# Kernel tuning notes

Measured on AMD Instinct MI355X. Metric: run time of the kernel, lower is better.

## Reference

```python
import jax, jax.numpy as jnp
import numpy as np

B, S, H, D = 2, 8192, 16, 64
P = 8            # lsh_num_projs
BS = 256         # block_size
SAMP = 256       # sample_size


def _gray_perm(num_projs):
    # AngularLSH._unit_hamming_distance_array: maps bin ids to Gray-code order
    a = np.array([0, 1], dtype=np.int32)
    for _ in range(num_projs - 1):
        a = np.concatenate([a, np.flip(a) + a.shape[0]])
    return a

_PERM = jnp.asarray(_gray_perm(P))          # (2**P,)
_POW2 = jnp.asarray(2 ** np.arange(P), dtype=jnp.int32)


def setup_inputs() -> dict:
    rng = jax.random.key(0)
    k1, k2, k3, k4, k5 = jax.random.split(rng, 5)
    return {
        "query": jax.random.normal(k1, (B, S, H, D), jnp.float32),
        "key": jax.random.normal(k2, (B, S, H, D), jnp.float32),
        "value": jax.random.normal(k3, (B, S, H, D), jnp.float32),
        "proj_dir": jax.random.normal(k4, (D, P), jnp.float32),
        "sample_idx": jax.random.randint(k5, (B, H, SAMP), 0, S),
    }


def _lsh_hash(x, proj_dir):
    # x: (B,S,H,D) -> Gray-coded bucket ids (B,H,S)
    bits = (jnp.einsum("bshd,dp->bhsp", x, proj_dir) > 0).astype(jnp.int32)
    bins = (bits * _POW2).sum(-1)
    return _PERM[bins]


def _gather_seq(x, idx_bhs):
    # x: (B,S,H,...) gathered along seq by idx (B,H,S)
    idx = jnp.transpose(idx_bhs, (0, 2, 1))  # (B,S,H)
    if x.ndim == 4:
        idx = idx[..., None]
    return jnp.take_along_axis(x, idx, axis=1)


def reference(query, key, value, proj_dir, sample_idx):
    scale = 1.0 / float(np.sqrt(D))
    nb = S // BS

    # --- LSH sort of queries and keys (stable argsort over seq) ---
    q_sort = jnp.argsort(_lsh_hash(query, proj_dir), axis=2)   # (B,H,S)
    k_sort = jnp.argsort(_lsh_hash(key, proj_dir), axis=2)     # (B,H,S)

    q_s = _gather_seq(query, q_sort)   # (B,S,H,D)
    k_s = _gather_seq(key, k_sort)
    v_s = _gather_seq(value, k_sort)

    # --- block-diagonal attention in sorted order ---
    qb = q_s.reshape(B, nb, BS, H, D)
    kb = k_s.reshape(B, nb, BS, H, D)
    vb = v_s.reshape(B, nb, BS, H, D)
    s_blk = jnp.einsum("bnihd,bnjhd->bhnij", qb, kb) * scale   # (B,H,nb,BS,BS)
    lse_blk = jax.nn.logsumexp(s_blk, axis=-1)                 # (B,H,nb,BS)
    a_blk = jnp.einsum("bhnij,bnjhd->bnihd", jax.nn.softmax(s_blk, axis=-1), vb)
    a_blk = a_blk.reshape(B, S, H, D)                          # sorted order
    lse_blk = jnp.transpose(lse_blk, (0, 2, 3, 1)).reshape(B, S, H)

    # un-sort back to original query order
    q_inv = jnp.argsort(q_sort, axis=2)                        # inverse perm (B,H,S)
    a_blk = _gather_seq(a_blk, q_inv)                          # (B,S,H,D)
    lse_blk = _gather_seq(lse_blk, q_inv)                      # (B,S,H)

    # --- residual: uniform sampled-key attention with importance weight ---
    k_r = _gather_seq(key, sample_idx)                         # (B,SAMP,H,D)
    v_r = _gather_seq(value, sample_idx)
    s_r = jnp.einsum("bihd,bjhd->bhij", query, k_r) * scale    # (B,H,S,SAMP)
    lse_r = jax.nn.logsumexp(s_r, axis=-1) + jnp.log(S / SAMP) # (B,H,S)
    a_r = jnp.einsum("bhij,bjhd->bihd", jax.nn.softmax(s_r, axis=-1), v_r)
    lse_r = jnp.transpose(lse_r, (0, 2, 1))                    # (B,S,H)

    # --- combine block + residual estimates via log-sum-exp ---
    lse_t = jnp.logaddexp(lse_blk, lse_r)                      # (B,S,H)
    w_blk = jnp.exp(lse_blk - lse_t)[..., None]
    w_r = jnp.exp(lse_r - lse_t)[..., None]
    attn = a_blk * w_blk + a_r * w_r                           # (B,S,H,D)
    return attn
```

## Files before the change

kernel.cpp:

```cpp
#include <hip/hip_runtime.h>
#include <hip/hip_bf16.h>

#define B 2
#define S 8192
#define H 16
#define D 64
#define NB 32
#define BS 256
#define SAMP 256
#define BH (B*H)
#define BHS (B*H*S)
#define BSHD (B*S*H*D)
#define LOG32 3.4657359027997265f

typedef float f32x4 __attribute__((ext_vector_type(4)));
typedef short bf16x8 __attribute__((ext_vector_type(8)));

__device__ __forceinline__ unsigned short f2bf(float x) {
    unsigned int u = __builtin_bit_cast(unsigned int, x);
    u += 0x7fffu + ((u >> 16) & 1u);
    return (unsigned short)(u >> 16);
}
__device__ __forceinline__ unsigned int pack2(float a, float b) {
    return (unsigned int)f2bf(a) | ((unsigned int)f2bf(b) << 16);
}

__global__ __launch_bounds__(256) void k_prep(const float* __restrict__ q,
                                              const float* __restrict__ k,
                                              const float* __restrict__ v,
                                              const float* __restrict__ pd,
                                              int* __restrict__ hq,
                                              int* __restrict__ hk,
                                              unsigned short* __restrict__ qbf,
                                              unsigned short* __restrict__ kbf,
                                              unsigned short* __restrict__ vbf) {
    __shared__ float spd[D * 8];
    const int t = threadIdx.x;
    for (int i = t; i < D * 8; i += 256) spd[i] = pd[i];
    __syncthreads();

    const int sc = blockIdx.x & (NB - 1);
    const int bh = blockIdx.x >> 5;
    const int s  = sc * 256 + t;
    const int h  = bh & (H - 1), b = bh >> 4;
    const int base = ((b * S + s) * H + h) << 6;

    float dq[8], dk[8];
#pragma unroll
    for (int p = 0; p < 8; ++p) { dq[p] = 0.f; dk[p] = 0.f; }

#pragma unroll
    for (int i = 0; i < 8; ++i) {
        float4 x0 = ((const float4*)(q + base + i * 8))[0];
        float4 x1 = ((const float4*)(q + base + i * 8))[1];
        float4 y0 = ((const float4*)(k + base + i * 8))[0];
        float4 y1 = ((const float4*)(k + base + i * 8))[1];
#pragma unroll
        for (int p = 0; p < 8; ++p) {
            dq[p] += x0.x * spd[(8*i+0)*8+p] + x0.y * spd[(8*i+1)*8+p]
                   + x0.z * spd[(8*i+2)*8+p] + x0.w * spd[(8*i+3)*8+p]
                   + x1.x * spd[(8*i+4)*8+p] + x1.y * spd[(8*i+5)*8+p]
                   + x1.z * spd[(8*i+6)*8+p] + x1.w * spd[(8*i+7)*8+p];
            dk[p] += y0.x * spd[(8*i+0)*8+p] + y0.y * spd[(8*i+1)*8+p]
                   + y0.z * spd[(8*i+2)*8+p] + y0.w * spd[(8*i+3)*8+p]
                   + y1.x * spd[(8*i+4)*8+p] + y1.y * spd[(8*i+5)*8+p]
                   + y1.z * spd[(8*i+6)*8+p] + y1.w * spd[(8*i+7)*8+p];
        }
        uint4 uq, uk;
        uq.x = pack2(x0.x * 0.125f, x0.y * 0.125f);
        uq.y = pack2(x0.z * 0.125f, x0.w * 0.125f);
        uq.z = pack2(x1.x * 0.125f, x1.y * 0.125f);
        uq.w = pack2(x1.z * 0.125f, x1.w * 0.125f);
        uk.x = pack2(y0.x, y0.y); uk.y = pack2(y0.z, y0.w);
        uk.z = pack2(y1.x, y1.y); uk.w = pack2(y1.z, y1.w);
        *(uint4*)(qbf + base + i * 8) = uq;
        *(uint4*)(kbf + base + i * 8) = uk;

        float4 z0 = ((const float4*)(v + base + i * 8))[0];
        float4 z1 = ((const float4*)(v + base + i * 8))[1];
        uint4 uv;
        uv.x = pack2(z0.x, z0.y); uv.y = pack2(z0.z, z0.w);
        uv.z = pack2(z1.x, z1.y); uv.w = pack2(z1.z, z1.w);
        *(uint4*)(vbf + base + i * 8) = uv;
    }
    int bq = 0, bk = 0;
#pragma unroll
    for (int p = 0; p < 8; ++p) {
        bq |= (dq[p] > 0.f) ? (1 << p) : 0;
        bk |= (dk[p] > 0.f) ? (1 << p) : 0;
    }
    hq[bh * S + s] = bq ^ (bq >> 1);
    hk[bh * S + s] = bk ^ (bk >> 1);
}

#define SORT_NT 64
#define SORT_CH (S / SORT_NT)

__global__ __launch_bounds__(SORT_NT) void k_sort(const int* __restrict__ hq,
                                                  const int* __restrict__ hk,
                                                  int* __restrict__ qs,
                                                  int* __restrict__ ks) {
    __shared__ int hist[SORT_NT * 256];
    __shared__ int base[257];
    const int t  = threadIdx.x;
    const int bh = blockIdx.x & (BH - 1);
    const bool isQ = blockIdx.x < BH;
    const int* hp = (isQ ? hq : hk) + bh * S;
    int*       sp = (isQ ? qs : ks) + bh * S;

    for (int i = 0; i < 256; ++i) hist[t * 256 + i] = 0;
    __syncthreads();
    for (int i = 0; i < SORT_CH; ++i) hist[t * 256 + hp[t * SORT_CH + i]]++;
    __syncthreads();

    for (int bi = 0; bi < 4; ++bi) {
        const int bin = t * 4 + bi;
        int sum = 0;
        for (int tt = 0; tt < SORT_NT; ++tt) sum += hist[tt * 256 + bin];
        base[bin + 1] = sum;
    }
    __syncthreads();
    if (t == 0) {
        base[0] = 0;
        for (int i = 1; i <= 256; ++i) base[i] += base[i - 1];
    }
    __syncthreads();

    for (int bi = 0; bi < 4; ++bi) {
        const int bin = t * 4 + bi;
        int run = base[bin];
        for (int tt = 0; tt < SORT_NT; ++tt) {
            int c = hist[tt * 256 + bin];
            hist[tt * 256 + bin] = run;
            run += c;
        }
    }
    __syncthreads();

    for (int i = 0; i < SORT_CH; ++i) {
        const int s0  = t * SORT_CH + i;
        const int bin = hp[s0];
        sp[hist[t * 256 + bin]++] = s0;
    }
}

#define VP 264
#define PP 40

__global__ __launch_bounds__(512, 4) void k_attn(const unsigned short* __restrict__ qbf,
                                                 const unsigned short* __restrict__ kbf,
                                                 const unsigned short* __restrict__ vbf,
                                                 const int* __restrict__ qs,
                                                 const int* __restrict__ ks,
                                                 const int* __restrict__ sidx,
                                                 float* __restrict__ out) {
    __shared__ __align__(16) unsigned short vT[64 * VP];
    __shared__ __align__(16) unsigned short pL[8 * 32 * PP];

    const int t    = threadIdx.x;
    const int w    = t >> 6;
    const int lane = t & 63;
    const int lg   = lane >> 4;
    const int lr   = lane & 15;
    const int blk  = blockIdx.x & (NB - 1);
    const int bh   = blockIdx.x >> 5;
    const int h    = bh & (H - 1), b = bh >> 4;
    const int sbase = bh * S + blk * BS;
    unsigned short* pw = pL + w * 32 * PP;

    int qrow[2]; bf16x8 bq[2][2];
#pragma unroll
    for (int qg = 0; qg < 2; ++qg) {
        qrow[qg] = qs[sbase + w * 32 + qg * 16 + lr];
        const unsigned short* qp = qbf + (((b * S + qrow[qg]) * H + h) << 6);
        bq[qg][0] = *(const bf16x8*)(qp + lg * 8);
        bq[qg][1] = *(const bf16x8*)(qp + 32 + lg * 8);
    }

    float m_run[2] = {-1e30f, -1e30f}, l_run[2] = {0.f, 0.f};
    f32x4 acc[2][4];
#pragma unroll
    for (int qg = 0; qg < 2; ++qg)
#pragma unroll
        for (int dg = 0; dg < 4; ++dg) acc[qg][dg] = (f32x4){0.f, 0.f, 0.f, 0.f};

    for (int pass = 0; pass < 2; ++pass) {
        if (pass) __syncthreads();
        {
            const int key = t >> 1, d0 = (t & 1) * 32;
            const int krow = pass ? sidx[bh * SAMP + key] : ks[sbase + key];
            const unsigned short* vp = vbf + (((b * S + krow) * H + h) << 6) + d0;
#pragma unroll
            for (int i = 0; i < 4; ++i) {
                uint4 x = *(const uint4*)(vp + i * 8);
                const int d = d0 + i * 8;
                vT[(d + 0) * VP + key] = (unsigned short)(x.x);
                vT[(d + 1) * VP + key] = (unsigned short)(x.x >> 16);
                vT[(d + 2) * VP + key] = (unsigned short)(x.y);
                vT[(d + 3) * VP + key] = (unsigned short)(x.y >> 16);
                vT[(d + 4) * VP + key] = (unsigned short)(x.z);
                vT[(d + 5) * VP + key] = (unsigned short)(x.z >> 16);
                vT[(d + 6) * VP + key] = (unsigned short)(x.w);
                vT[(d + 7) * VP + key] = (unsigned short)(x.w >> 16);
            }
        }
        __syncthreads();

        const float bias = pass ? LOG32 : 0.f;
        for (int kt4 = 0; kt4 < 4; ++kt4) {
            int krw[4];
#pragma unroll
            for (int kg = 0; kg < 4; ++kg) {
                const int key = kt4 * 64 + kg * 16 + lr;
                krw[kg] = pass ? sidx[bh * SAMP + key] : ks[sbase + key];
            }
            f32x4 c[2][4];
#pragma unroll
            for (int kf = 0; kf < 2; ++kf) {
                bf16x8 ak[4];
#pragma unroll
                for (int kg = 0; kg < 4; ++kg)
                    ak[kg] = *(const bf16x8*)(kbf + (((b * S + krw[kg]) * H + h) << 6)
                                              + kf * 32 + lg * 8);
#pragma unroll
                for (int qg = 0; qg < 2; ++qg)
#pragma unroll
                    for (int kg = 0; kg < 4; ++kg) {
                        f32x4 cin = kf ? c[qg][kg] : (f32x4){0.f, 0.f, 0.f, 0.f};
                        c[qg][kg] = __builtin_amdgcn_mfma_f32_16x16x32_bf16(ak[kg], bq[qg][kf], cin, 0, 0, 0);
                    }
            }
            float esc[2];
#pragma unroll
            for (int qg = 0; qg < 2; ++qg) {
                float tm = -1e30f;
#pragma unroll
                for (int kg = 0; kg < 4; ++kg)
#pragma unroll
                    for (int r = 0; r < 4; ++r) tm = fmaxf(tm, c[qg][kg][r]);
                tm = fmaxf(tm, __shfl_xor(tm, 16));
                tm = fmaxf(tm, __shfl_xor(tm, 32));
                tm += bias;
                const float mn = fmaxf(m_run[qg], tm);
                esc[qg] = __expf(m_run[qg] - mn);
                m_run[qg] = mn;
                const float mnb = mn - bias;
                float rs = 0.f;
#pragma unroll
                for (int kg = 0; kg < 4; ++kg)
#pragma unroll
                    for (int r = 0; r < 4; ++r) {
                        const float p = __expf(c[qg][kg][r] - mnb);
                        c[qg][kg][r] = p;
                        rs += p;
                    }
                rs += __shfl_xor(rs, 16);
                rs += __shfl_xor(rs, 32);
                l_run[qg] = l_run[qg] * esc[qg] + rs;
            }
#pragma unroll
            for (int qg = 0; qg < 2; ++qg)
#pragma unroll
                for (int r = 0; r < 4; ++r) {
                    const float er = __shfl(esc[qg], lg * 4 + r);
#pragma unroll
                    for (int dg = 0; dg < 4; ++dg) acc[qg][dg][r] *= er;
                }
#pragma unroll
            for (int hh = 0; hh < 2; ++hh) {
#pragma unroll
                for (int qg = 0; qg < 2; ++qg)
#pragma unroll
                    for (int kg2 = 0; kg2 < 2; ++kg2) {
                        const int kg = hh * 2 + kg2;
                        uint2 u;
                        u.x = pack2(c[qg][kg][0], c[qg][kg][1]);
                        u.y = pack2(c[qg][kg][2], c[qg][kg][3]);
                        *(uint2*)&pw[(qg * 16 + lr) * PP + kg2 * 16 + lg * 4] = u;
                    }
                bf16x8 bv[4];
#pragma unroll
                for (int dg = 0; dg < 4; ++dg)
                    bv[dg] = *(const bf16x8*)&vT[(dg * 16 + lr) * VP + kt4 * 64 + hh * 32 + lg * 8];
#pragma unroll
                for (int qg = 0; qg < 2; ++qg) {
                    const bf16x8 ap = *(const bf16x8*)&pw[(qg * 16 + lr) * PP + lg * 8];
#pragma unroll
                    for (int dg = 0; dg < 4; ++dg)
                        acc[qg][dg] = __builtin_amdgcn_mfma_f32_16x16x32_bf16(ap, bv[dg], acc[qg][dg], 0, 0, 0);
                }
            }
        }
    }

#pragma unroll
    for (int qg = 0; qg < 2; ++qg)
#pragma unroll
        for (int r = 0; r < 4; ++r) {
            const float lq = __shfl(l_run[qg], lg * 4 + r);
            const int   qr = __shfl(qrow[qg], lg * 4 + r);
            const float inv = 1.f / lq;
            const int obase = ((b * S + qr) * H + h) << 6;
#pragma unroll
            for (int dg = 0; dg < 4; ++dg)
                out[obase + dg * 16 + lr] = acc[qg][dg][r] * inv;
        }
}

extern "C" void kernel_launch(void* const* d_in, const int* in_sizes, int n_in,
                              void* d_out, int out_size, void* d_ws, size_t ws_size,
                              hipStream_t stream) {
    const float* q   = (const float*)d_in[0];
    const float* k   = (const float*)d_in[1];
    const float* v   = (const float*)d_in[2];
    const float* pd  = (const float*)d_in[3];
    const int*  sidx = (const int*)d_in[4];
    float* out = (float*)d_out;

    int* hq = (int*)d_ws;
    int* hk = hq + BHS;
    int* qs = hk + BHS;
    int* ks = qs + BHS;
    unsigned short* qbf = (unsigned short*)(ks + BHS);
    unsigned short* kbf = qbf + BSHD;
    unsigned short* vbf = kbf + BSHD;

    k_prep<<<BH * NB, 256, 0, stream>>>(q, k, v, pd, hq, hk, qbf, kbf, vbf);
    k_sort<<<2 * BH, SORT_NT, 0, stream>>>(hq, hk, qs, ks);
    k_attn<<<BH * NB, 512, 0, stream>>>(qbf, kbf, vbf, qs, ks, sidx, out);
}
```

Baseline: 230.4 us.

## Drop bf16 query staging, remap prep threads, lazy rescale, swizzle attention blocks

After: 379.4 us. 1.65x slower.

```diff
diff --git a/kernel.cpp b/kernel.cpp
--- a/kernel.cpp
+++ b/kernel.cpp
@@ -25,25 +25,25 @@
     return (unsigned int)f2bf(a) | ((unsigned int)f2bf(b) << 16);
 }
 
-__global__ __launch_bounds__(256) void k_prep(const float* __restrict__ q,
-                                              const float* __restrict__ k,
-                                              const float* __restrict__ v,
-                                              const float* __restrict__ pd,
-                                              int* __restrict__ hq,
-                                              int* __restrict__ hk,
-                                              unsigned short* __restrict__ qbf,
-                                              unsigned short* __restrict__ kbf,
-                                              unsigned short* __restrict__ vbf) {
+__global__ __launch_bounds__(256, 3) void k_prep(const float* __restrict__ q,
+                                                 const float* __restrict__ k,
+                                                 const float* __restrict__ v,
+                                                 const float* __restrict__ pd,
+                                                 int* __restrict__ hq,
+                                                 int* __restrict__ hk,
+                                                 unsigned short* __restrict__ kbf,
+                                                 unsigned short* __restrict__ vbf) {
     __shared__ float spd[D * 8];
+    __shared__ int   ht[2][16][16];
     const int t = threadIdx.x;
     for (int i = t; i < D * 8; i += 256) spd[i] = pd[i];
     __syncthreads();
 
-    const int sc = blockIdx.x & (NB - 1);
-    const int bh = blockIdx.x >> 5;
-    const int s  = sc * 256 + t;
-    const int h  = bh & (H - 1), b = bh >> 4;
-    const int base = ((b * S + s) * H + h) << 6;
+    const int b  = blockIdx.x >> 9;
+    const int s0 = (blockIdx.x & 511) * 16;
+    const int sl = t >> 4;
+    const int h  = t & 15;
+    const int base = ((b * S + s0 + sl) * H + h) << 6;
 
     float dq[8], dk[8];
 #pragma unroll
@@ -53,29 +53,26 @@
     for (int i = 0; i < 8; ++i) {
         float4 x0 = ((const float4*)(q + base + i * 8))[0];
         float4 x1 = ((const float4*)(q + base + i * 8))[1];
-        float4 y0 = ((const float4*)(k + base + i * 8))[0];
-        float4 y1 = ((const float4*)(k + base + i * 8))[1];
 #pragma unroll
         for (int p = 0; p < 8; ++p) {
             dq[p] += x0.x * spd[(8*i+0)*8+p] + x0.y * spd[(8*i+1)*8+p]
                    + x0.z * spd[(8*i+2)*8+p] + x0.w * spd[(8*i+3)*8+p]
                    + x1.x * spd[(8*i+4)*8+p] + x1.y * spd[(8*i+5)*8+p]
                    + x1.z * spd[(8*i+6)*8+p] + x1.w * spd[(8*i+7)*8+p];
+        }
+        float4 y0 = ((const float4*)(k + base + i * 8))[0];
+        float4 y1 = ((const float4*)(k + base + i * 8))[1];
+#pragma unroll
+        for (int p = 0; p < 8; ++p) {
             dk[p] += y0.x * spd[(8*i+0)*8+p] + y0.y * spd[(8*i+1)*8+p]
                    + y0.z * spd[(8*i+2)*8+p] + y0.w * spd[(8*i+3)*8+p]
                    + y1.x * spd[(8*i+4)*8+p] + y1.y * spd[(8*i+5)*8+p]
                    + y1.z * spd[(8*i+6)*8+p] + y1.w * spd[(8*i+7)*8+p];
         }
-        uint4 uq, uk;
-        uq.x = pack2(x0.x * 0.125f, x0.y * 0.125f);
-        uq.y = pack2(x0.z * 0.125f, x0.w * 0.125f);
-        uq.z = pack2(x1.x * 0.125f, x1.y * 0.125f);
-        uq.w = pack2(x1.z * 0.125f, x1.w * 0.125f);
+        uint4 uk;
         uk.x = pack2(y0.x, y0.y); uk.y = pack2(y0.z, y0.w);
         uk.z = pack2(y1.x, y1.y); uk.w = pack2(y1.z, y1.w);
-        *(uint4*)(qbf + base + i * 8) = uq;
         *(uint4*)(kbf + base + i * 8) = uk;
-
         float4 z0 = ((const float4*)(v + base + i * 8))[0];
         float4 z1 = ((const float4*)(v + base + i * 8))[1];
         uint4 uv;
@@ -89,8 +86,16 @@
         bq |= (dq[p] > 0.f) ? (1 << p) : 0;
         bk |= (dk[p] > 0.f) ? (1 << p) : 0;
     }
-    hq[bh * S + s] = bq ^ (bq >> 1);
-    hk[bh * S + s] = bk ^ (bk >> 1);
+    ht[0][h][sl] = bq ^ (bq >> 1);
+    ht[1][h][sl] = bk ^ (bk >> 1);
+    __syncthreads();
+
+    if (t < 128) {
+        const int inp = t >> 6, r = t & 63, h2 = r >> 2, p2 = r & 3;
+        int4 val = *(const int4*)&ht[inp][h2][p2 * 4];
+        int* dst = inp ? hk : hq;
+        *(int4*)&dst[(b * H + h2) * S + s0 + p2 * 4] = val;
+    }
 }
 
 #define SORT_NT 64
@@ -147,7 +152,7 @@
 #define VP 264
 #define PP 40
 
-__global__ __launch_bounds__(512, 4) void k_attn(const unsigned short* __restrict__ qbf,
+__global__ __launch_bounds__(512, 4) void k_attn(const float* __restrict__ q,
                                                  const unsigned short* __restrict__ kbf,
                                                  const unsigned short* __restrict__ vbf,
                                                  const int* __restrict__ qs,
@@ -162,8 +167,9 @@
     const int lane = t & 63;
     const int lg   = lane >> 4;
     const int lr   = lane & 15;
-    const int blk  = blockIdx.x & (NB - 1);
-    const int bh   = blockIdx.x >> 5;
+    const int logical = (blockIdx.x & 7) * (BH * NB / 8) + (blockIdx.x >> 3);
+    const int blk  = logical & (NB - 1);
+    const int bh   = logical >> 5;
     const int h    = bh & (H - 1), b = bh >> 4;
     const int sbase = bh * S + blk * BS;
     unsigned short* pw = pL + w * 32 * PP;
@@ -172,9 +178,18 @@
 #pragma unroll
     for (int qg = 0; qg < 2; ++qg) {
         qrow[qg] = qs[sbase + w * 32 + qg * 16 + lr];
-        const unsigned short* qp = qbf + (((b * S + qrow[qg]) * H + h) << 6);
-        bq[qg][0] = *(const bf16x8*)(qp + lg * 8);
-        bq[qg][1] = *(const bf16x8*)(qp + 32 + lg * 8);
+        const float* qp = q + (((b * S + qrow[qg]) * H + h) << 6);
+#pragma unroll
+        for (int kf = 0; kf < 2; ++kf) {
+            float4 x0 = ((const float4*)(qp + kf * 32 + lg * 8))[0];
+            float4 x1 = ((const float4*)(qp + kf * 32 + lg * 8))[1];
+            union { bf16x8 v8; unsigned int u[4]; } fa;
+            fa.u[0] = pack2(x0.x * 0.125f, x0.y * 0.125f);
+            fa.u[1] = pack2(x0.z * 0.125f, x0.w * 0.125f);
+            fa.u[2] = pack2(x1.x * 0.125f, x1.y * 0.125f);
+            fa.u[3] = pack2(x1.z * 0.125f, x1.w * 0.125f);
+            bq[qg][kf] = fa.v8;
+        }
     }
 
     float m_run[2] = {-1e30f, -1e30f}, l_run[2] = {0.f, 0.f};
@@ -230,7 +245,6 @@
                         c[qg][kg] = __builtin_amdgcn_mfma_f32_16x16x32_bf16(ak[kg], bq[qg][kf], cin, 0, 0, 0);
                     }
             }
-            float esc[2];
 #pragma unroll
             for (int qg = 0; qg < 2; ++qg) {
                 float tm = -1e30f;
@@ -241,10 +255,19 @@
                 tm = fmaxf(tm, __shfl_xor(tm, 16));
                 tm = fmaxf(tm, __shfl_xor(tm, 32));
                 tm += bias;
-                const float mn = fmaxf(m_run[qg], tm);
-                esc[qg] = __expf(m_run[qg] - mn);
-                m_run[qg] = mn;
-                const float mnb = mn - bias;
+                if (!__all(tm <= m_run[qg] + 8.f)) {
+                    const float mn  = fmaxf(m_run[qg], tm);
+                    const float es  = __expf(m_run[qg] - mn);
+                    m_run[qg] = mn;
+                    l_run[qg] *= es;
+#pragma unroll
+                    for (int r = 0; r < 4; ++r) {
+                        const float er = __shfl(es, lg * 4 + r);
+#pragma unroll
+                        for (int dg = 0; dg < 4; ++dg) acc[qg][dg][r] *= er;
+                    }
+                }
+                const float mnb = m_run[qg] - bias;
                 float rs = 0.f;
 #pragma unroll
                 for (int kg = 0; kg < 4; ++kg)
@@ -256,16 +279,8 @@
                     }
                 rs += __shfl_xor(rs, 16);
                 rs += __shfl_xor(rs, 32);
-                l_run[qg] = l_run[qg] * esc[qg] + rs;
-            }
-#pragma unroll
-            for (int qg = 0; qg < 2; ++qg)
-#pragma unroll
-                for (int r = 0; r < 4; ++r) {
-                    const float er = __shfl(esc[qg], lg * 4 + r);
-#pragma unroll
-                    for (int dg = 0; dg < 4; ++dg) acc[qg][dg][r] *= er;
-                }
+                l_run[qg] += rs;
+            }
 #pragma unroll
             for (int hh = 0; hh < 2; ++hh) {
 #pragma unroll
@@ -321,11 +336,10 @@
     int* hk = hq + BHS;
     int* qs = hk + BHS;
     int* ks = qs + BHS;
-    unsigned short* qbf = (unsigned short*)(ks + BHS);
-    unsigned short* kbf = qbf + BSHD;
+    unsigned short* kbf = (unsigned short*)(ks + BHS);
     unsigned short* vbf = kbf + BSHD;
 
-    k_prep<<<BH * NB, 256, 0, stream>>>(q, k, v, pd, hq, hk, qbf, kbf, vbf);
+    k_prep<<<B * (S / 16), 256, 0, stream>>>(q, k, v, pd, hq, hk, kbf, vbf);
     k_sort<<<2 * BH, SORT_NT, 0, stream>>>(hq, hk, qs, ks);
-    k_attn<<<BH * NB, 512, 0, stream>>>(qbf, kbf, vbf, qs, ks, sidx, out);
-}
+    k_attn<<<BH * NB, 512, 0, stream>>>(q, kbf, vbf, qs, ks, sidx, out);
+}
```
